# Kernel optimization log

Measured on AMD Instinct MI355X. Metric: run time of the kernel, lower is better.

Reference implementation:

```python
import jax, jax.numpy as jnp
import numpy as np

B, S, D = 8, 512, 768
HEADS = 16           # label_n
HD = 64              # size_per_head
NEG = 1e12


def setup_inputs() -> dict:
    key = jax.random.key(0)
    k1, k2, k3 = jax.random.split(key, 3)
    hidden = jax.random.normal(k1, (B, S, D), dtype=jnp.float32)
    token_ids = jax.random.randint(k2, (B, S), 0, 21128, dtype=jnp.int32)
    W = jax.random.normal(k3, (D, HEADS * 2 * HD), dtype=jnp.float32) * 0.02
    b = jnp.zeros((HEADS * 2 * HD,), dtype=jnp.float32)
    return {"hidden": hidden, "token_ids": token_ids, "W": W, "b": b}


def _rope(x):
    # x: [B, S, H, HD] -> RoPE-rotated, Su Jianlin interleaved convention
    d = x.shape[-1]
    inv_freq = 1.0 / (10000.0 ** (jnp.arange(0, d, 2, dtype=jnp.float32) / d))  # [d/2]
    pos = jnp.arange(x.shape[1], dtype=jnp.float32)                              # [S]
    freqs = pos[:, None] * inv_freq[None, :]                                     # [S, d/2]
    sin = jnp.repeat(jnp.sin(freqs), 2, axis=-1)[None, :, None, :]               # [1,S,1,d]
    cos = jnp.repeat(jnp.cos(freqs), 2, axis=-1)[None, :, None, :]
    x2 = jnp.stack([-x[..., 1::2], x[..., 0::2]], axis=-1).reshape(x.shape)
    return x * cos + x2 * sin


def reference(hidden, token_ids, W, b):
    # qk projection: [B,S,H,2,HD]
    qk = (hidden @ W + b).reshape(B, S, HEADS, 2, HD)
    q, k = qk[..., 0, :], qk[..., 1, :]          # [B,S,H,HD]
    q = _rope(q)
    k = _rope(k)
    # all-pairs span scores per entity head
    logits = jnp.einsum('bmhd,bnhd->bhmn', q, k) / jnp.sqrt(jnp.float32(HD))
    # padding mask from token ids (0 = pad)
    mask = (token_ids > 0).astype(logits.dtype)  # [B,S]
    logits = logits - (1.0 - mask[:, None, :, None]) * NEG
    logits = logits - (1.0 - mask[:, None, None, :]) * NEG
    # strict lower-triangular mask (spans must have start <= end)
    tril = jnp.tril(jnp.ones((S, S), dtype=logits.dtype), k=-1)
    logits = logits - tril[None, None, :, :] * NEG
    # valid-span weight mask (upper triangle incl. diag, both positions valid)
    tri_mask = (1.0 - tril)[None, None, :, :] * mask[:, None, :, None] * mask[:, None, None, :]
    return logits, tri_mask
```

## Files before the change

### kernel.cpp

```cpp
#include <hip/hip_runtime.h>
#include <hip/hip_bf16.h>
#include <cstdint>
#include <cstddef>


#define NEGV 1.0e12f

typedef short bf16x8 __attribute__((ext_vector_type(8)));
typedef float f32x4  __attribute__((ext_vector_type(4)));

static __device__ __forceinline__ short f2b(float x) {
    __hip_bfloat16 h = __float2bfloat16(x);
    union { __hip_bfloat16 h; short s; } u; u.h = h; return u.s;
}
static __device__ __forceinline__ float b2f(short s) {
    union { short s; __hip_bfloat16 h; } u; u.s = s; return __bfloat162float(u.h);
}

static __device__ __forceinline__ void gload16(const short* g, short* l) {
    __builtin_amdgcn_global_load_lds(
        (const __attribute__((address_space(1))) void*)g,
        (__attribute__((address_space(3))) void*)l, 16, 0, 0);
}

__global__ __launch_bounds__(256) void prep_kernel(const float* __restrict__ hidden,
                                                   short* __restrict__ Xb,
                                                   float* __restrict__ SinT,
                                                   float* __restrict__ CosT) {
    int t = blockIdx.x * 256 + threadIdx.x;
    if (t < 393216) {
        const float4* hp = (const float4*)hidden;
        float4 a = hp[t * 2];
        float4 c = hp[t * 2 + 1];
        bf16x8 v;
        v[0] = f2b(a.x); v[1] = f2b(a.y); v[2] = f2b(a.z); v[3] = f2b(a.w);
        v[4] = f2b(c.x); v[5] = f2b(c.y); v[6] = f2b(c.z); v[7] = f2b(c.w);
        *(bf16x8*)(Xb + t * 8) = v;
    } else if (t < 393216 + 16384) {
        int u = t - 393216;
        int s = u >> 5, i = u & 31;
        float ang = (float)s * exp2f(-0.4152410118609203f * (float)i);
        float sn, cs;
        __sincosf(ang, &sn, &cs);
        SinT[u] = sn;
        CosT[u] = cs;
    }
}

__global__ __launch_bounds__(256) void transpose_w(const float* __restrict__ W,
                                                   short* __restrict__ Wt) {
    __shared__ short T[64 * 68];
    int k0 = (blockIdx.x % 12) * 64;
    int n0 = (blockIdx.x / 12) * 64;
    int tid = threadIdx.x;

    int r = tid >> 2;
    int cbase = (tid & 3) * 4;
#pragma unroll
    for (int q = 0; q < 4; ++q) {
        int c = cbase + q * 16;
        float4 v = *(const float4*)(W + (size_t)(k0 + r) * 2048 + n0 + c);
        short* tp = T + r * 68 + c;
        tp[0] = f2b(v.x); tp[1] = f2b(v.y); tp[2] = f2b(v.z); tp[3] = f2b(v.w);
    }
    __syncthreads();

    int n = tid >> 2;
    int kc = (tid & 3) * 16;
    bf16x8 o0, o1;
#pragma unroll
    for (int j = 0; j < 8; ++j) {
        o0[j] = T[(kc + j) * 68 + n];
        o1[j] = T[(kc + 8 + j) * 68 + n];
    }
    short* wp = Wt + (size_t)(n0 + n) * 768 + k0 + kc;
    *(bf16x8*)wp       = o0;
    *(bf16x8*)(wp + 8) = o1;
}

__global__ __launch_bounds__(256) void gemm_qk(const short* __restrict__ A,
                                               const short* __restrict__ Bt,
                                               const float* __restrict__ bias,
                                               short* __restrict__ C) {
    __shared__ short As[128 * 32];
    __shared__ short Bs[128 * 32];
    const int m0 = (blockIdx.x >> 4) * 128;
    const int n0 = (blockIdx.x & 15) * 128;
    const int tid  = threadIdx.x;
    const int wave = tid >> 6, lane = tid & 63;
    const int quad = lane >> 4, r16 = lane & 15;
    const int wm = (wave >> 1) * 64, wn = (wave & 1) * 64;

    const int srow = wave * 32 + (lane >> 2);
    const int scol = (lane & 3) * 8;
    const short* gA0 = A  + (size_t)(m0 + srow) * 768 + scol;
    const short* gA1 = gA0 + 16 * 768;
    const short* gB0 = Bt + (size_t)(n0 + srow) * 768 + scol;
    const short* gB1 = gB0 + 16 * 768;
    short* lA0 = As + (wave * 32) * 32;
    short* lA1 = As + (wave * 32 + 16) * 32;
    short* lB0 = Bs + (wave * 32) * 32;
    short* lB1 = Bs + (wave * 32 + 16) * 32;

    f32x4 acc[4][4] = {};

    for (int k0 = 0; k0 < 768; k0 += 32) {
        __syncthreads();
        gload16(gA0 + k0, lA0);
        gload16(gA1 + k0, lA1);
        gload16(gB0 + k0, lB0);
        gload16(gB1 + k0, lB1);
        __syncthreads();

        bf16x8 af[4], bfr[4];
#pragma unroll
        for (int mi = 0; mi < 4; ++mi)
            af[mi] = *(const bf16x8*)(As + (wm + mi * 16 + r16) * 32 + quad * 8);
#pragma unroll
        for (int ni = 0; ni < 4; ++ni)
            bfr[ni] = *(const bf16x8*)(Bs + (wn + ni * 16 + r16) * 32 + quad * 8);
#pragma unroll
        for (int mi = 0; mi < 4; ++mi)
#pragma unroll
            for (int ni = 0; ni < 4; ++ni)
                acc[mi][ni] = __builtin_amdgcn_mfma_f32_16x16x32_bf16(
                    af[mi], bfr[ni], acc[mi][ni], 0, 0, 0);
    }

#pragma unroll
    for (int mi = 0; mi < 4; ++mi)
#pragma unroll
        for (int ni = 0; ni < 4; ++ni) {
            int col = n0 + wn + ni * 16 + r16;
            float bv = bias[col];
            int rowb = m0 + wm + mi * 16 + quad * 4;
#pragma unroll
            for (int r = 0; r < 4; ++r)
                C[(size_t)(rowb + r) * 2048 + col] = f2b(acc[mi][ni][r] + bv);
        }
}

__global__ __launch_bounds__(256) void logits_kernel(const short* __restrict__ QKi,
                                                     const float* __restrict__ SinT,
                                                     const float* __restrict__ CosT,
                                                     const int* __restrict__ tok,
                                                     float* __restrict__ out,
                                                     float* __restrict__ out2) {
    __shared__ short Qs[128 * 72];
    __shared__ short Ks[128 * 72];
    __shared__ float rowNeg[128];
    __shared__ float colNeg[128];

    int blk = blockIdx.x;
    int nt = blk & 3, mt = (blk >> 2) & 3, bh = blk >> 4;
    int b = bh >> 4, h = bh & 15;
    int m0 = mt * 128, n0 = nt * 128;

    const int tid  = threadIdx.x;
    const int wave = tid >> 6, lane = tid & 63;
    const int quad = lane >> 4, r16 = lane & 15;
    const int wm = (wave >> 1) * 64, wn = (wave & 1) * 64;

    int row = tid >> 1;
    int ch  = (tid & 1) * 32;
    int sQ = m0 + row, sK = n0 + row;
    const short* qsrc = QKi + ((size_t)(b * 512 + sQ)) * 2048 + h * 128 + ch;
    const short* ksrc = QKi + ((size_t)(b * 512 + sK)) * 2048 + h * 128 + 64 + ch;
    const float* sQs = SinT + sQ * 32;  const float* sQc = CosT + sQ * 32;
    const float* sKs = SinT + sK * 32;  const float* sKc = CosT + sK * 32;

#pragma unroll
    for (int j = 0; j < 4; ++j) {
        int i0 = (ch >> 1) + j * 4;
        bf16x8 v = *(const bf16x8*)(qsrc + j * 8);
        f32x4 sn = *(const f32x4*)(sQs + i0);
        f32x4 cs = *(const f32x4*)(sQc + i0);
        bf16x8 o;
#pragma unroll
        for (int p = 0; p < 4; ++p) {
            float f0 = b2f(v[2 * p]), f1 = b2f(v[2 * p + 1]);
            o[2 * p]     = f2b(f0 * cs[p] - f1 * sn[p]);
            o[2 * p + 1] = f2b(f1 * cs[p] + f0 * sn[p]);
        }
        *(bf16x8*)(Qs + row * 72 + ch + j * 8) = o;
        v  = *(const bf16x8*)(ksrc + j * 8);
        sn = *(const f32x4*)(sKs + i0);
        cs = *(const f32x4*)(sKc + i0);
#pragma unroll
        for (int p = 0; p < 4; ++p) {
            float f0 = b2f(v[2 * p]), f1 = b2f(v[2 * p + 1]);
            o[2 * p]     = f2b(f0 * cs[p] - f1 * sn[p]);
            o[2 * p + 1] = f2b(f1 * cs[p] + f0 * sn[p]);
        }
        *(bf16x8*)(Ks + row * 72 + ch + j * 8) = o;
    }
    if (tid < 128)        rowNeg[tid]       = (tok[b * 512 + m0 + tid] > 0) ? 0.f : NEGV;
    else if (tid < 256)   colNeg[tid - 128] = (tok[b * 512 + n0 + (tid - 128)] > 0) ? 0.f : NEGV;
    __syncthreads();

    f32x4 acc[4][4] = {};
#pragma unroll
    for (int kk = 0; kk < 64; kk += 32) {
        bf16x8 af[4], bfr[4];
#pragma unroll
        for (int mi = 0; mi < 4; ++mi)
            af[mi] = *(const bf16x8*)(Qs + (wm + mi * 16 + r16) * 72 + kk + quad * 8);
#pragma unroll
        for (int ni = 0; ni < 4; ++ni)
            bfr[ni] = *(const bf16x8*)(Ks + (wn + ni * 16 + r16) * 72 + kk + quad * 8);
#pragma unroll
        for (int mi = 0; mi < 4; ++mi)
#pragma unroll
            for (int ni = 0; ni < 4; ++ni)
                acc[mi][ni] = __builtin_amdgcn_mfma_f32_16x16x32_bf16(
                    af[mi], bfr[ni], acc[mi][ni], 0, 0, 0);
    }

    float* obase = out + (size_t)bh * 512 * 512;
#pragma unroll
    for (int mi = 0; mi < 4; ++mi)
#pragma unroll
        for (int ni = 0; ni < 4; ++ni) {
            int n = n0 + wn + ni * 16 + r16;
            float cn = colNeg[n - n0];
#pragma unroll
            for (int r = 0; r < 4; ++r) {
                int m = m0 + wm + mi * 16 + quad * 4 + r;
                float v = acc[mi][ni][r] * 0.125f - rowNeg[m - m0] - cn
                          - ((m > n) ? NEGV : 0.0f);
                obase[(size_t)m * 512 + n] = v;
            }
        }

    if (h == 0) {
        float* o2 = out2 + (size_t)b * 512 * 512;
#pragma unroll
        for (int mi = 0; mi < 4; ++mi)
#pragma unroll
            for (int ni = 0; ni < 4; ++ni) {
                int n = n0 + wn + ni * 16 + r16;
                float mn = (colNeg[n - n0] == 0.f) ? 1.f : 0.f;
#pragma unroll
                for (int r = 0; r < 4; ++r) {
                    int m = m0 + wm + mi * 16 + quad * 4 + r;
                    float mm = (rowNeg[m - m0] == 0.f) ? 1.f : 0.f;
                    o2[(size_t)m * 512 + n] = (m > n) ? 0.f : (mm * mn);
                }
            }
    }
}

extern "C" void kernel_launch(void* const* d_in, const int* in_sizes, int n_in,
                              void* d_out, int out_size, void* d_ws, size_t ws_size,
                              hipStream_t stream) {
    const float* hidden = (const float*)d_in[0];
    const int*   tok    = (const int*)d_in[1];
    const float* W      = (const float*)d_in[2];
    const float* bias   = (const float*)d_in[3];
    float* out  = (float*)d_out;
    float* out2 = out + 33554432;

    char* ws = (char*)d_ws;
    short* QKi  = (short*)(ws);
    short* Xb   = (short*)(ws + 16777216);
    short* Wt   = (short*)(ws + 23068672);
    float* SinT = (float*)(ws + 26214400);
    float* CosT = (float*)(ws + 26279936);

    hipLaunchKernelGGL(prep_kernel,   dim3(1600), dim3(256), 0, stream, hidden, Xb, SinT, CosT);
    hipLaunchKernelGGL(transpose_w,   dim3(384),  dim3(256), 0, stream, W, Wt);
    hipLaunchKernelGGL(gemm_qk,       dim3(512),  dim3(256), 0, stream, Xb, Wt, bias, QKi);
    hipLaunchKernelGGL(logits_kernel, dim3(2048), dim3(256), 0, stream, QKi, SinT, CosT, tok, out, out2);
}
```

Baseline: 198.8 us.

## Fuse RoPE into GEMM epilogue, merge prep kernels, swizzle LDS layouts

The W transpose is merged into the prep kernel, removing one launch. RoPE and bias are now applied in the QK GEMM epilogue using lane shuffles, and results are written as head-major Q and K buffers. The logits kernel then loads pre-rotated tiles straight into LDS with direct global-to-LDS loads. Both the GEMM and logits LDS layouts use XOR swizzles to avoid bank conflicts without padding. The GEMM epilogue now does scattered 2-byte stores plus sin/cos table lookups, which may cost more than the old per-row rotation.

```diff
diff --git a/kernel.cpp b/kernel.cpp
--- a/kernel.cpp
+++ b/kernel.cpp
@@ -16,7 +16,6 @@
 static __device__ __forceinline__ float b2f(short s) {
     union { short s; __hip_bfloat16 h; } u; u.s = s; return __bfloat162float(u.h);
 }
-
 static __device__ __forceinline__ void gload16(const short* g, short* l) {
     __builtin_amdgcn_global_load_lds(
         (const __attribute__((address_space(1))) void*)g,
@@ -24,64 +23,59 @@
 }
 
 __global__ __launch_bounds__(256) void prep_kernel(const float* __restrict__ hidden,
+                                                   const float* __restrict__ W,
                                                    short* __restrict__ Xb,
+                                                   short* __restrict__ Wt,
                                                    float* __restrict__ SinT,
                                                    float* __restrict__ CosT) {
-    int t = blockIdx.x * 256 + threadIdx.x;
-    if (t < 393216) {
+    __shared__ short T[64 * 68];
+    int blk = blockIdx.x, tid = threadIdx.x;
+    if (blk < 1536) {
+        int t = blk * 256 + tid;
         const float4* hp = (const float4*)hidden;
-        float4 a = hp[t * 2];
-        float4 c = hp[t * 2 + 1];
+        float4 a = hp[t * 2], c = hp[t * 2 + 1];
         bf16x8 v;
         v[0] = f2b(a.x); v[1] = f2b(a.y); v[2] = f2b(a.z); v[3] = f2b(a.w);
         v[4] = f2b(c.x); v[5] = f2b(c.y); v[6] = f2b(c.z); v[7] = f2b(c.w);
         *(bf16x8*)(Xb + t * 8) = v;
-    } else if (t < 393216 + 16384) {
-        int u = t - 393216;
+    } else if (blk < 1600) {
+        int u = (blk - 1536) * 256 + tid;
         int s = u >> 5, i = u & 31;
         float ang = (float)s * exp2f(-0.4152410118609203f * (float)i);
-        float sn, cs;
-        __sincosf(ang, &sn, &cs);
-        SinT[u] = sn;
-        CosT[u] = cs;
-    }
-}
-
-__global__ __launch_bounds__(256) void transpose_w(const float* __restrict__ W,
-                                                   short* __restrict__ Wt) {
-    __shared__ short T[64 * 68];
-    int k0 = (blockIdx.x % 12) * 64;
-    int n0 = (blockIdx.x / 12) * 64;
-    int tid = threadIdx.x;
-
-    int r = tid >> 2;
-    int cbase = (tid & 3) * 4;
-#pragma unroll
-    for (int q = 0; q < 4; ++q) {
-        int c = cbase + q * 16;
-        float4 v = *(const float4*)(W + (size_t)(k0 + r) * 2048 + n0 + c);
-        short* tp = T + r * 68 + c;
-        tp[0] = f2b(v.x); tp[1] = f2b(v.y); tp[2] = f2b(v.z); tp[3] = f2b(v.w);
-    }
-    __syncthreads();
-
-    int n = tid >> 2;
-    int kc = (tid & 3) * 16;
-    bf16x8 o0, o1;
-#pragma unroll
-    for (int j = 0; j < 8; ++j) {
-        o0[j] = T[(kc + j) * 68 + n];
-        o1[j] = T[(kc + 8 + j) * 68 + n];
-    }
-    short* wp = Wt + (size_t)(n0 + n) * 768 + k0 + kc;
-    *(bf16x8*)wp       = o0;
-    *(bf16x8*)(wp + 8) = o1;
-}
-
-__global__ __launch_bounds__(256) void gemm_qk(const short* __restrict__ A,
-                                               const short* __restrict__ Bt,
-                                               const float* __restrict__ bias,
-                                               short* __restrict__ C) {
+        float sn, cs; __sincosf(ang, &sn, &cs);
+        SinT[u] = sn; CosT[u] = cs;
+    } else {
+        int tb = blk - 1600;
+        int k0 = (tb % 12) * 64, n0 = (tb / 12) * 64;
+        int r = tid >> 2, cb = (tid & 3) * 4;
+#pragma unroll
+        for (int q = 0; q < 4; ++q) {
+            int c = cb + q * 16;
+            float4 v = *(const float4*)(W + (size_t)(k0 + r) * 2048 + n0 + c);
+            short* tp = T + r * 68 + c;
+            tp[0] = f2b(v.x); tp[1] = f2b(v.y); tp[2] = f2b(v.z); tp[3] = f2b(v.w);
+        }
+        __syncthreads();
+        int n = tid >> 2, kc = (tid & 3) * 16;
+        bf16x8 o0, o1;
+#pragma unroll
+        for (int j = 0; j < 8; ++j) {
+            o0[j] = T[(kc + j) * 68 + n];
+            o1[j] = T[(kc + 8 + j) * 68 + n];
+        }
+        short* wp = Wt + (size_t)(n0 + n) * 768 + k0 + kc;
+        *(bf16x8*)wp = o0;
+        *(bf16x8*)(wp + 8) = o1;
+    }
+}
+
+__global__ __launch_bounds__(256) void gemm_rope(const short* __restrict__ A,
+                                                 const short* __restrict__ Bt,
+                                                 const float* __restrict__ bias,
+                                                 const float* __restrict__ SinT,
+                                                 const float* __restrict__ CosT,
+                                                 short* __restrict__ Qb,
+                                                 short* __restrict__ Kb) {
     __shared__ short As[128 * 32];
     __shared__ short Bs[128 * 32];
     const int m0 = (blockIdx.x >> 4) * 128;
@@ -91,19 +85,20 @@
     const int quad = lane >> 4, r16 = lane & 15;
     const int wm = (wave >> 1) * 64, wn = (wave & 1) * 64;
 
-    const int srow = wave * 32 + (lane >> 2);
-    const int scol = (lane & 3) * 8;
-    const short* gA0 = A  + (size_t)(m0 + srow) * 768 + scol;
-    const short* gA1 = gA0 + 16 * 768;
-    const short* gB0 = Bt + (size_t)(n0 + srow) * 768 + scol;
-    const short* gB1 = gB0 + 16 * 768;
-    short* lA0 = As + (wave * 32) * 32;
-    short* lA1 = As + (wave * 32 + 16) * 32;
-    short* lB0 = Bs + (wave * 32) * 32;
-    short* lB1 = Bs + (wave * 32 + 16) * 32;
+    const int swc = ((lane & 3) ^ ((lane >> 3) & 3)) * 8;
+    const int r0  = wave * 32 + (lane >> 2);
+    const short* gA0 = A  + (size_t)(m0 + r0) * 768 + swc;
+    const short* gA1 = A  + (size_t)(m0 + r0 + 16) * 768 + swc;
+    const short* gB0 = Bt + (size_t)(n0 + r0) * 768 + swc;
+    const short* gB1 = Bt + (size_t)(n0 + r0 + 16) * 768 + swc;
+    short* lA0 = As + wave * 1024;
+    short* lA1 = As + wave * 1024 + 512;
+    short* lB0 = Bs + wave * 1024;
+    short* lB1 = Bs + wave * 1024 + 512;
+
+    const int sw16 = (r16 >> 1) & 3;
 
     f32x4 acc[4][4] = {};
-
     for (int k0 = 0; k0 < 768; k0 += 32) {
         __syncthreads();
         gload16(gA0 + k0, lA0);
@@ -115,10 +110,10 @@
         bf16x8 af[4], bfr[4];
 #pragma unroll
         for (int mi = 0; mi < 4; ++mi)
-            af[mi] = *(const bf16x8*)(As + (wm + mi * 16 + r16) * 32 + quad * 8);
+            af[mi] = *(const bf16x8*)(As + (wm + mi * 16 + r16) * 32 + (quad ^ sw16) * 8);
 #pragma unroll
         for (int ni = 0; ni < 4; ++ni)
-            bfr[ni] = *(const bf16x8*)(Bs + (wn + ni * 16 + r16) * 32 + quad * 8);
+            bfr[ni] = *(const bf16x8*)(Bs + (wn + ni * 16 + r16) * 32 + (quad ^ sw16) * 8);
 #pragma unroll
         for (int mi = 0; mi < 4; ++mi)
 #pragma unroll
@@ -127,27 +122,39 @@
                     af[mi], bfr[ni], acc[mi][ni], 0, 0, 0);
     }
 
-#pragma unroll
-    for (int mi = 0; mi < 4; ++mi)
-#pragma unroll
-        for (int ni = 0; ni < 4; ++ni) {
-            int col = n0 + wn + ni * 16 + r16;
-            float bv = bias[col];
-            int rowb = m0 + wm + mi * 16 + quad * 4;
-#pragma unroll
-            for (int r = 0; r < 4; ++r)
-                C[(size_t)(rowb + r) * 2048 + col] = f2b(acc[mi][ni][r] + bv);
-        }
-}
-
-__global__ __launch_bounds__(256) void logits_kernel(const short* __restrict__ QKi,
-                                                     const float* __restrict__ SinT,
-                                                     const float* __restrict__ CosT,
+    const int b     = m0 >> 9;
+    const int s0l   = (m0 & 511) + wm + quad * 4;
+    const int h     = n0 >> 7;
+    const int which = wn >> 6;
+    short* dstT = (which ? Kb : Qb) + (size_t)(b * 16 + h) * 512 * 64;
+    const float sgn = (r16 & 1) ? 1.0f : -1.0f;
+#pragma unroll
+    for (int ni = 0; ni < 4; ++ni) {
+        int col = n0 + wn + ni * 16 + r16;
+        float bv = bias[col];
+        int d  = ni * 16 + r16;
+        int ii = d >> 1;
+#pragma unroll
+        for (int mi = 0; mi < 4; ++mi)
+#pragma unroll
+            for (int r = 0; r < 4; ++r) {
+                int s = s0l + mi * 16 + r;
+                float v  = acc[mi][ni][r] + bv;
+                float pv = __shfl_xor(v, 1);
+                float sn = SinT[s * 32 + ii];
+                float cs = CosT[s * 32 + ii];
+                dstT[(size_t)s * 64 + d] = f2b(v * cs + sgn * pv * sn);
+            }
+    }
+}
+
+__global__ __launch_bounds__(256) void logits_kernel(const short* __restrict__ Qb,
+                                                     const short* __restrict__ Kb,
                                                      const int* __restrict__ tok,
                                                      float* __restrict__ out,
                                                      float* __restrict__ out2) {
-    __shared__ short Qs[128 * 72];
-    __shared__ short Ks[128 * 72];
+    __shared__ short Qs[128 * 64];
+    __shared__ short Ks[128 * 64];
     __shared__ float rowNeg[128];
     __shared__ float colNeg[128];
 
@@ -161,53 +168,34 @@
     const int quad = lane >> 4, r16 = lane & 15;
     const int wm = (wave >> 1) * 64, wn = (wave & 1) * 64;
 
-    int row = tid >> 1;
-    int ch  = (tid & 1) * 32;
-    int sQ = m0 + row, sK = n0 + row;
-    const short* qsrc = QKi + ((size_t)(b * 512 + sQ)) * 2048 + h * 128 + ch;
-    const short* ksrc = QKi + ((size_t)(b * 512 + sK)) * 2048 + h * 128 + 64 + ch;
-    const float* sQs = SinT + sQ * 32;  const float* sQc = CosT + sQ * 32;
-    const float* sKs = SinT + sK * 32;  const float* sKc = CosT + sK * 32;
-
-#pragma unroll
-    for (int j = 0; j < 4; ++j) {
-        int i0 = (ch >> 1) + j * 4;
-        bf16x8 v = *(const bf16x8*)(qsrc + j * 8);
-        f32x4 sn = *(const f32x4*)(sQs + i0);
-        f32x4 cs = *(const f32x4*)(sQc + i0);
-        bf16x8 o;
-#pragma unroll
-        for (int p = 0; p < 4; ++p) {
-            float f0 = b2f(v[2 * p]), f1 = b2f(v[2 * p + 1]);
-            o[2 * p]     = f2b(f0 * cs[p] - f1 * sn[p]);
-            o[2 * p + 1] = f2b(f1 * cs[p] + f0 * sn[p]);
-        }
-        *(bf16x8*)(Qs + row * 72 + ch + j * 8) = o;
-        v  = *(const bf16x8*)(ksrc + j * 8);
-        sn = *(const f32x4*)(sKs + i0);
-        cs = *(const f32x4*)(sKc + i0);
-#pragma unroll
-        for (int p = 0; p < 4; ++p) {
-            float f0 = b2f(v[2 * p]), f1 = b2f(v[2 * p + 1]);
-            o[2 * p]     = f2b(f0 * cs[p] - f1 * sn[p]);
-            o[2 * p + 1] = f2b(f1 * cs[p] + f0 * sn[p]);
-        }
-        *(bf16x8*)(Ks + row * 72 + ch + j * 8) = o;
-    }
-    if (tid < 128)        rowNeg[tid]       = (tok[b * 512 + m0 + tid] > 0) ? 0.f : NEGV;
-    else if (tid < 256)   colNeg[tid - 128] = (tok[b * 512 + n0 + (tid - 128)] > 0) ? 0.f : NEGV;
+    const short* gsrc = (wave < 2)
+        ? Qb + ((size_t)bh * 512 + m0) * 64
+        : Kb + ((size_t)bh * 512 + n0) * 64;
+    short* ldst = (wave < 2) ? Qs : Ks;
+    const int wv = wave & 1;
+    const int gc = ((lane & 7) ^ (lane >> 3)) * 8;
+    const int rl = wv * 64 + (lane >> 3);
+#pragma unroll
+    for (int j = 0; j < 8; ++j)
+        gload16(gsrc + (rl + j * 8) * 64 + gc, ldst + wv * 4096 + j * 512);
+
+    if (tid < 128)      rowNeg[tid]       = (tok[b * 512 + m0 + tid] > 0) ? 0.f : NEGV;
+    else if (tid < 256) colNeg[tid - 128] = (tok[b * 512 + n0 + (tid - 128)] > 0) ? 0.f : NEGV;
     __syncthreads();
 
+    const int sw8 = r16 & 7;
     f32x4 acc[4][4] = {};
 #pragma unroll
-    for (int kk = 0; kk < 64; kk += 32) {
+    for (int kb = 0; kb < 2; ++kb) {
         bf16x8 af[4], bfr[4];
 #pragma unroll
         for (int mi = 0; mi < 4; ++mi)
-            af[mi] = *(const bf16x8*)(Qs + (wm + mi * 16 + r16) * 72 + kk + quad * 8);
+            af[mi] = *(const bf16x8*)(Qs + (wm + mi * 16 + r16) * 64
+                                         + ((quad + kb * 4) ^ sw8) * 8);
 #pragma unroll
         for (int ni = 0; ni < 4; ++ni)
-            bfr[ni] = *(const bf16x8*)(Ks + (wn + ni * 16 + r16) * 72 + kk + quad * 8);
+            bfr[ni] = *(const bf16x8*)(Ks + (wn + ni * 16 + r16) * 64
+                                          + ((quad + kb * 4) ^ sw8) * 8);
 #pragma unroll
         for (int mi = 0; mi < 4; ++mi)
 #pragma unroll
@@ -261,14 +249,17 @@
     float* out2 = out + 33554432;
 
     char* ws = (char*)d_ws;
-    short* QKi  = (short*)(ws);
-    short* Xb   = (short*)(ws + 16777216);
-    short* Wt   = (short*)(ws + 23068672);
-    float* SinT = (float*)(ws + 26214400);
-    float* CosT = (float*)(ws + 26279936);
-
-    hipLaunchKernelGGL(prep_kernel,   dim3(1600), dim3(256), 0, stream, hidden, Xb, SinT, CosT);
-    hipLaunchKernelGGL(transpose_w,   dim3(384),  dim3(256), 0, stream, W, Wt);
-    hipLaunchKernelGGL(gemm_qk,       dim3(512),  dim3(256), 0, stream, Xb, Wt, bias, QKi);
-    hipLaunchKernelGGL(logits_kernel, dim3(2048), dim3(256), 0, stream, QKi, SinT, CosT, tok, out, out2);
-}
+    short* Xb   = (short*)(ws);
+    short* Wt   = (short*)(ws + 6291456);
+    float* SinT = (float*)(ws + 9437184);
+    float* CosT = (float*)(ws + 9502720);
+    short* Qb   = (short*)(ws + 9568256);
+    short* Kb   = (short*)(ws + 17956864);
+
+    hipLaunchKernelGGL(prep_kernel,   dim3(1984), dim3(256), 0, stream,
+                       hidden, W, Xb, Wt, SinT, CosT);
+    hipLaunchKernelGGL(gemm_rope,     dim3(512),  dim3(256), 0, stream,
+                       Xb, Wt, bias, SinT, CosT, Qb, Kb);
+    hipLaunchKernelGGL(logits_kernel, dim3(2048), dim3(256), 0, stream,
+                       Qb, Kb, tok, out, out2);
+}
```

After: 189.1 us. 4.9% less time.
